# Optimization experiments

Hardware: AMD Instinct MI355X
Metric: run time of the kernel (lower is better)

Reference implementation:

```python
import jax, jax.numpy as jnp
import numpy as np

FILTER_SIZE = 4  # DAIN default filter_size


def _grid(H, W, dtype):
    Y, X = jnp.meshgrid(jnp.arange(H, dtype=dtype), jnp.arange(W, dtype=dtype), indexing='ij')
    return X, Y


def depth_flow_project(flow, depth_inv):
    """DepthFlowProjectionModule: forward-splat -flow, weighted by inverse depth,
    onto the 4 integer neighbors of the flow target, then normalize.
    flow: (B,2,H,W), depth_inv: (B,1,H,W) -> (B,2,H,W) projected flow at time t."""
    B, _, H, W = flow.shape
    X, Y = _grid(H, W, flow.dtype)
    x2 = X[None] + flow[:, 0]
    y2 = Y[None] + flow[:, 1]
    xL = jnp.floor(x2).astype(jnp.int32)
    yT = jnp.floor(y2).astype(jnp.int32)
    d = depth_inv[:, 0]                                            # (B,H,W)
    b_off = (jnp.arange(B, dtype=jnp.int32) * (H * W))[:, None, None]
    fvals = jnp.stack([flow[:, 0], flow[:, 1]], axis=-1).reshape(-1, 2)  # (BHW,2)
    acc = jnp.zeros((B * H * W, 2), flow.dtype)
    cnt = jnp.zeros((B * H * W,), flow.dtype)
    for dy in (0, 1):
        for dx in (0, 1):
            xi = xL + dx
            yi = yT + dy
            valid = (xi >= 0) & (xi < W) & (yi >= 0) & (yi < H)
            idx = (b_off + jnp.clip(yi, 0, H - 1) * W + jnp.clip(xi, 0, W - 1)).reshape(-1)
            w = jnp.where(valid, d, 0.0).reshape(-1)
            acc = acc.at[idx].add(-fvals * w[:, None])
            cnt = cnt.at[idx].add(w)
    cnt_safe = jnp.where(cnt > 0, cnt, 1.0)
    out = jnp.where((cnt > 0)[:, None], acc / cnt_safe[:, None], 0.0)
    return out.reshape(B, H, W, 2).transpose(0, 3, 1, 2)


def _gather(imf, idx, H, W):
    # imf: (B,C,H*W), idx: (B,H,W) int32 -> (B,C,H,W)
    B, C, _ = imf.shape
    g = jax.vmap(lambda m, i: m[:, i])(imf, idx.reshape(B, -1))
    return g.reshape(B, C, H, W)


def filter_interpolate(im, offset, filt):
    """FilterInterpolationModule: per-pixel 4x4 adaptive filter applied at the
    backward-warp location x+u, y+v; each tap is sampled bilinearly at
    (x2 + fi - 1, y2 + fj - 1) and weighted by filt[:, fj*4+fi]."""
    B, C, H, W = im.shape
    X, Y = _grid(H, W, im.dtype)
    x2 = X[None] + offset[:, 0]
    y2 = Y[None] + offset[:, 1]
    valid = (x2 >= 0) & (x2 <= W - 1) & (y2 >= 0) & (y2 <= H - 1)
    xLf = jnp.floor(x2)
    yTf = jnp.floor(y2)
    alpha = (x2 - xLf)[:, None]                                    # (B,1,H,W)
    beta = (y2 - yTf)[:, None]
    xL = xLf.astype(jnp.int32)
    yT = yTf.astype(jnp.int32)
    imf = im.reshape(B, C, H * W)
    half = FILTER_SIZE // 2 - 1  # = 1: window starts at floor - 1
    acc = jnp.zeros_like(im)
    for fj in range(FILTER_SIZE):
        for fi in range(FILTER_SIZE):
            xi = jnp.clip(xL + fi - half, 0, W - 1)
            yi = jnp.clip(yT + fj - half, 0, H - 1)
            xi1 = jnp.clip(xi + 1, 0, W - 1)
            yi1 = jnp.clip(yi + 1, 0, H - 1)
            tl = _gather(imf, yi * W + xi, H, W)
            tr = _gather(imf, yi * W + xi1, H, W)
            bl = _gather(imf, yi1 * W + xi, H, W)
            br = _gather(imf, yi1 * W + xi1, H, W)
            samp = ((1 - alpha) * (1 - beta) * tl + alpha * (1 - beta) * tr
                    + (1 - alpha) * beta * bl + alpha * beta * br)
            acc = acc + filt[:, fj * FILTER_SIZE + fi][:, None] * samp
    return jnp.where(valid[:, None], acc, 0.0)


def setup_inputs() -> dict:
    key = jax.random.key(0)
    ks = jax.random.split(key, 10)
    B, H, W = 2, 192, 320
    CTX = 3 * 64 + 3  # ctx_ch hardcoded in DAIN.__init__
    im0 = jax.random.uniform(ks[0], (B, 3, H, W), jnp.float32)
    im2 = jax.random.uniform(ks[1], (B, 3, H, W), jnp.float32)
    ctx0 = jax.random.normal(ks[2], (B, CTX, H, W), jnp.float32)
    ctx2 = jax.random.normal(ks[3], (B, CTX, H, W), jnp.float32)
    flow01 = jax.random.normal(ks[4], (B, 2, H, W), jnp.float32) * 4.0
    flow10 = jax.random.normal(ks[5], (B, 2, H, W), jnp.float32) * 4.0
    depth0_inv = jax.random.uniform(ks[6], (B, 1, H, W), jnp.float32) + 1e-6
    depth1_inv = jax.random.uniform(ks[7], (B, 1, H, W), jnp.float32) + 1e-6
    filt0 = jax.random.uniform(ks[8], (B, FILTER_SIZE ** 2, H, W), jnp.float32)
    filt1 = jax.random.uniform(ks[9], (B, FILTER_SIZE ** 2, H, W), jnp.float32)
    return {"im0": im0, "im2": im2, "ctx0": ctx0, "ctx2": ctx2,
            "flow01": flow01, "flow10": flow10,
            "depth0_inv": depth0_inv, "depth1_inv": depth1_inv,
            "filt0": filt0, "filt1": filt1}


def reference(im0, im2, ctx0, ctx2, flow01, flow10, depth0_inv, depth1_inv, filt0, filt1):
    # STEP: FlowProject (depth-aware forward warping of the PWC flows to time t)
    off0 = depth_flow_project(flow01, depth0_inv)
    off1 = depth_flow_project(flow10, depth1_inv)
    # STEP: FilterInterpolate on frames (adaptive-filter backward warp) + blend
    ref0 = filter_interpolate(im0, off0, filt0)
    ref2 = filter_interpolate(im2, off1, filt1)
    cur_output = ref0 / 2.0 + ref2 / 2.0
    # STEP: FilterInterpolate_ctx on context features (offsets/filters detached in torch)
    ctx0_w = filter_interpolate(ctx0, jax.lax.stop_gradient(off0), jax.lax.stop_gradient(filt0))
    ctx2_w = filter_interpolate(ctx2, jax.lax.stop_gradient(off1), jax.lax.stop_gradient(filt1))
    return (cur_output, ref0, ref2, ctx0_w, ctx2_w, off0, off1)
```

## Files before the change

### kernel.cpp

```cpp
#include <hip/hip_runtime.h>
#include <hip/hip_fp16.h>
#include <math.h>

#define B   2
#define H   192
#define W   320
#define HW  (H * W)
#define BHW (B * HW)
#define CTX 195
#define CH  198

#define OFS_CUR   0
#define OFS_REF0  (3 * BHW)
#define OFS_REF2  (6 * BHW)
#define OFS_CTX0  (9 * BHW)
#define OFS_CTX2  (9 * BHW + CTX * BHW)
#define OFS_OFF0  (9 * BHW + 2 * CTX * BHW)
#define OFS_OFF1  (OFS_OFF0 + 2 * BHW)

#define TSZ    ((size_t)2 * B * HW * CH)
#define NTB    (2 * B * (HW / 64))
#define LDSW   199
#define NPXB   32
#define NTHR   512
#define NCHK   (HW / NPXB)
#define NBLK2  (2 * B * NCHK)

#define F_NCH   33
#define F_NGRP  6
#define F_TX    32
#define F_TY    8
#define F_NTX   (W / F_TX)
#define F_NTY   (H / F_TY)
#define F_NTILE (F_NTX * F_NTY * B)
#define F_NBLK  (F_NTILE * F_NGRP * 2)

typedef float f4a __attribute__((ext_vector_type(4), aligned(4)));
typedef _Float16 h4 __attribute__((ext_vector_type(4), aligned(4)));

__device__ __forceinline__ int iclip(int v, int lo, int hi) {
    return v < lo ? lo : (v > hi ? hi : v);
}


__global__ __launch_bounds__(256) void splat_kernel(
    const float* __restrict__ flow0, const float* __restrict__ flow1,
    const float* __restrict__ dep0,  const float* __restrict__ dep1,
    float* __restrict__ acc4)
{
    int tid = blockIdx.x * blockDim.x + threadIdx.x;
    if (tid >= 2 * BHW) return;
    int s   = tid / BHW;
    int p   = tid - s * BHW;
    int b   = p / HW;
    int pix = p - b * HW;
    int y   = pix / W;
    int x   = pix - y * W;

    const float* flow = s ? flow1 : flow0;
    const float* dep  = s ? dep1  : dep0;
    float fx = flow[(b * 2 + 0) * HW + pix];
    float fy = flow[(b * 2 + 1) * HW + pix];
    float d  = dep[b * HW + pix];

    int xL = (int)floorf((float)x + fx);
    int yT = (int)floorf((float)y + fy);

    float* ab = acc4 + (size_t)(s * B + b) * HW * 4;

    float wx = -fx * d;
    float wy = -fy * d;
    #pragma unroll
    for (int dy = 0; dy < 2; dy++) {
        #pragma unroll
        for (int dx = 0; dx < 2; dx++) {
            int xi = xL + dx;
            int yi = yT + dy;
            if (xi >= 0 && xi < W && yi >= 0 && yi < H) {
                float* q = ab + (size_t)(yi * W + xi) * 4;
                atomicAdd(q + 0, wx);
                atomicAdd(q + 1, wy);
                atomicAdd(q + 2, d);
            }
        }
    }
}

__global__ __launch_bounds__(256) void norm_kernel(
    float* __restrict__ out, const float* __restrict__ acc4)
{
    int tid = blockIdx.x * blockDim.x + threadIdx.x;
    if (tid >= 2 * BHW) return;
    int s   = tid / BHW;
    int p   = tid - s * BHW;
    int b   = p / HW;
    int pix = p - b * HW;

    const float* q = acc4 + ((size_t)(s * B + b) * HW + pix) * 4;
    float ax = q[0], ay = q[1], c = q[2];
    float* acc = out + (s ? OFS_OFF1 : OFS_OFF0) + b * 2 * HW;
    if (c > 0.0f) {
        acc[pix]      = ax / c;
        acc[HW + pix] = ay / c;
    } else {
        acc[pix]      = 0.0f;
        acc[HW + pix] = 0.0f;
    }
}

__global__ __launch_bounds__(256) void cur_kernel(float* __restrict__ out)
{
    int i = blockIdx.x * blockDim.x + threadIdx.x;
    if (i < 3 * BHW)
        out[OFS_CUR + i] = 0.5f * (out[OFS_REF0 + i] + out[OFS_REF2 + i]);
}


__global__ __launch_bounds__(256) void transpose_kernel(
    const float* __restrict__ im0,  const float* __restrict__ im2,
    const float* __restrict__ ctx0, const float* __restrict__ ctx2,
    _Float16* __restrict__ T)
{
    __shared__ float lds[64 * LDSW];
    int lin   = blockIdx.x;
    int chunk = lin % (HW / 64);
    int rest  = lin / (HW / 64);
    int b = rest % B;
    int s = rest / B;
    int pix0 = chunk * 64;

    const float* im  = s ? im2  : im0;
    const float* ctx = s ? ctx2 : ctx0;

    for (int j = (int)threadIdx.x; j < CH * 64; j += 256) {
        int c = j >> 6;
        int p = j & 63;
        const float* src = (c < 3) ? im + (b * 3 + c) * HW
                                   : ctx + (b * CTX + (c - 3)) * HW;
        lds[p * LDSW + c] = src[pix0 + p];
    }
    __syncthreads();
    _Float16* Tb = T + ((size_t)((s * B + b) * HW + pix0)) * CH;
    for (int j = (int)threadIdx.x; j < CH * 64; j += 256) {
        int p = j / CH;
        int c = j - p * CH;
        Tb[(size_t)p * CH + c] = (_Float16)lds[p * LDSW + c];
    }
}

__global__ __launch_bounds__(NTHR) void interp_t_kernel(
    const _Float16* __restrict__ T,
    const float* __restrict__ filt0, const float* __restrict__ filt1,
    float* __restrict__ out)
{
    __shared__ float fwl[NPXB * 17];
    __shared__ float mwl[NPXB * 25];
    __shared__ float geof[NPXB * 6];
    __shared__ int   geoi[NPXB * 4];
    __shared__ float outb[NPXB * 199];

    int lin = blockIdx.x;
    int newlin = (lin & 7) * (NBLK2 / 8) + (lin >> 3);
    int chunk = newlin % NCHK;
    int rest  = newlin / NCHK;
    int b = rest % B;
    int s = rest / B;
    int px0 = chunk * NPXB;
    int y0  = px0 / W;
    int x0  = px0 - y0 * W;

    const float* off  = out + (s ? OFS_OFF1 : OFS_OFF0) + b * 2 * HW;
    const float* filt = (s ? filt1 : filt0) + b * 16 * HW;
    const _Float16* Tb = T + (size_t)(s * B + b) * HW * CH;

    int t = (int)threadIdx.x;

    for (int idx = t; idx < 16 * NPXB; idx += NTHR) {
        int tap = idx >> 5, p = idx & 31;
        fwl[p * 17 + tap] = filt[tap * HW + px0 + p];
    }
    if (t < NPXB) {
        int p = t;
        float ox = off[px0 + p];
        float oy = off[HW + px0 + p];
        float x2 = (float)(x0 + p) + ox;
        float y2 = (float)y0 + oy;
        bool valid = (x2 >= 0.0f) && (x2 <= (float)(W - 1)) &&
                     (y2 >= 0.0f) && (y2 <= (float)(H - 1));
        float xLf = floorf(x2), yTf = floorf(y2);
        float al = x2 - xLf, be = y2 - yTf;
        int xL = (int)xLf, yT = (int)yTf;
        bool interior = valid && (xL >= 1) && (xL <= W - 4) &&
                                 (yT >= 1) && (yT <= H - 4);
        geof[p * 6 + 0] = valid ? (1.0f - al) * (1.0f - be) : 0.0f;
        geof[p * 6 + 1] = valid ? al * (1.0f - be) : 0.0f;
        geof[p * 6 + 2] = valid ? (1.0f - al) * be : 0.0f;
        geof[p * 6 + 3] = valid ? al * be : 0.0f;
        geoi[p * 4 + 0] = valid ? (interior ? 1 : 2) : 0;
        geoi[p * 4 + 1] = xL;
        geoi[p * 4 + 2] = yT;
    }
    __syncthreads();
    for (int idx = t; idx < 25 * NPXB; idx += NTHR) {
        int p = idx / 25, rc = idx - p * 25;
        int r = rc / 5, c = rc - r * 5;
        float a00 = geof[p * 6 + 0], a10 = geof[p * 6 + 1];
        float a01 = geof[p * 6 + 2], a11 = geof[p * 6 + 3];
        const float* fw = &fwl[p * 17];
        float v = 0.0f;
        if (r < 4 && c < 4)   v += a00 * fw[r * 4 + c];
        if (r < 4 && c >= 1)  v += a10 * fw[r * 4 + c - 1];
        if (r >= 1 && c < 4)  v += a01 * fw[(r - 1) * 4 + c];
        if (r >= 1 && c >= 1) v += a11 * fw[(r - 1) * 4 + c - 1];
        mwl[p * 25 + rc] = v;
    }
    __syncthreads();

    int wave = t >> 6, lane = t & 63;
    int lcl = lane < 49 ? lane : 49;
    int cc0 = 4 * lcl;
    int nwr = lane < 49 ? 4 : (lane == 49 ? 2 : 0);

    #pragma unroll
    for (int pi = 0; pi < 4; pi++) {
        int p = wave * 4 + pi;
        int flag = geoi[p * 4];
        float acc0 = 0.0f, acc1 = 0.0f, acc2 = 0.0f, acc3 = 0.0f;
        if (flag == 1) {
            int xL = geoi[p * 4 + 1], yT = geoi[p * 4 + 2];
            const _Float16* basep =
                Tb + ((size_t)(yT - 1) * W + (xL - 1)) * CH + cc0;
            #pragma unroll
            for (int r = 0; r < 5; r++) {
                #pragma unroll
                for (int cc = 0; cc < 5; cc++) {
                    h4 v = *(const h4*)(basep + ((size_t)r * W + cc) * CH);
                    float wgt = mwl[p * 25 + r * 5 + cc];
                    acc0 = fmaf(wgt, (float)v.x, acc0);
                    acc1 = fmaf(wgt, (float)v.y, acc1);
                    acc2 = fmaf(wgt, (float)v.z, acc2);
                    acc3 = fmaf(wgt, (float)v.w, acc3);
                }
            }
        } else if (flag == 2) {
            int xL = geoi[p * 4 + 1], yT = geoi[p * 4 + 2];
            float a00 = geof[p * 6 + 0], a10 = geof[p * 6 + 1];
            float a01 = geof[p * 6 + 2], a11 = geof[p * 6 + 3];
            int xi[4], xi1[4], yi[4], yi1[4];
            #pragma unroll
            for (int f = 0; f < 4; f++) {
                int a = iclip(xL + f - 1, 0, W - 1);
                xi[f]  = a;
                xi1[f] = a + 1 > W - 1 ? W - 1 : a + 1;
                int bb = iclip(yT + f - 1, 0, H - 1);
                yi[f]  = bb;
                yi1[f] = bb + 1 > H - 1 ? H - 1 : bb + 1;
            }
            #pragma unroll
            for (int fj = 0; fj < 4; fj++) {
                #pragma unroll
                for (int fi = 0; fi < 4; fi++) {
                    const _Float16* ptl = Tb + ((size_t)yi[fj]  * W + xi[fi])  * CH + cc0;
                    const _Float16* ptr_ = Tb + ((size_t)yi[fj]  * W + xi1[fi]) * CH + cc0;
                    const _Float16* pbl = Tb + ((size_t)yi1[fj] * W + xi[fi])  * CH + cc0;
                    const _Float16* pbr = Tb + ((size_t)yi1[fj] * W + xi1[fi]) * CH + cc0;
                    h4 tl = *(const h4*)ptl;
                    h4 tr = *(const h4*)ptr_;
                    h4 bl = *(const h4*)pbl;
                    h4 br = *(const h4*)pbr;
                    float wgt = fwl[p * 17 + fj * 4 + fi];
                    acc0 = fmaf(wgt, a00*(float)tl.x + a10*(float)tr.x + a01*(float)bl.x + a11*(float)br.x, acc0);
                    acc1 = fmaf(wgt, a00*(float)tl.y + a10*(float)tr.y + a01*(float)bl.y + a11*(float)br.y, acc1);
                    acc2 = fmaf(wgt, a00*(float)tl.z + a10*(float)tr.z + a01*(float)bl.z + a11*(float)br.z, acc2);
                    acc3 = fmaf(wgt, a00*(float)tl.w + a10*(float)tr.w + a01*(float)bl.w + a11*(float)br.w, acc3);
                }
            }
        }
        float* ob = &outb[p * 199 + cc0];
        if (nwr == 4) { ob[0] = acc0; ob[1] = acc1; ob[2] = acc2; ob[3] = acc3; }
        else if (nwr == 2) { ob[0] = acc0; ob[1] = acc1; }
    }

    __syncthreads();
    for (int idx = t; idx < CH * NPXB; idx += NTHR) {
        int c = idx >> 5;
        int p = idx & 31;
        float v = outb[p * 199 + c];
        if (c < 3)
            out[(s ? OFS_REF2 : OFS_REF0) + (b * 3 + c) * HW + px0 + p] = v;
        else
            __builtin_nontemporal_store(
                v, &out[(s ? OFS_CTX2 : OFS_CTX0) + (b * CTX + (c - 3)) * HW + px0 + p]);
    }
}


#define VBODY(PLANE, STORE)                                            \
    {                                                                  \
        const float* p0 = (PLANE) + base;                              \
        float acc = 0.0f;                                              \
        _Pragma("unroll")                                              \
        for (int r = 0; r < 5; r++) {                                  \
            const float* row = p0 + r * W;                             \
            f4a v0 = *(const f4a*)row;                                 \
            float v4 = row[4];                                         \
            acc = fmaf(mw[r][0], v0.x, acc);                           \
            acc = fmaf(mw[r][1], v0.y, acc);                           \
            acc = fmaf(mw[r][2], v0.z, acc);                           \
            acc = fmaf(mw[r][3], v0.w, acc);                           \
            acc = fmaf(mw[r][4], v4,   acc);                           \
        }                                                              \
        STORE;                                                         \
    }

#define BBODY(PLANE, STORE)                                            \
    {                                                                  \
        const float* plane = (PLANE);                                  \
        float acc = 0.0f;                                              \
        _Pragma("unroll")                                              \
        for (int fj = 0; fj < 4; fj++) {                               \
            const float* rT = plane + yi[fj]  * W;                     \
            const float* rB = plane + yi1[fj] * W;                     \
            _Pragma("unroll")                                          \
            for (int fi = 0; fi < 4; fi++) {                           \
                float samp = a00 * rT[xi[fi]] + a10 * rT[xi1[fi]]      \
                           + a01 * rB[xi[fi]] + a11 * rB[xi1[fi]];     \
                acc = fmaf(fw[fj * 4 + fi], samp, acc);                \
            }                                                          \
        }                                                              \
        STORE;                                                         \
    }

__global__ __launch_bounds__(256) void interp_f_kernel(
    const float* __restrict__ im0,   const float* __restrict__ im2,
    const float* __restrict__ ctx0,  const float* __restrict__ ctx2,
    const float* __restrict__ filt0, const float* __restrict__ filt1,
    float* __restrict__ out)
{
    int lin = blockIdx.x + F_NTILE * (blockIdx.y + F_NGRP * blockIdx.z);
    int newlin = (lin & 7) * (F_NBLK / 8) + (lin >> 3);
    int tile = newlin % F_NTILE;
    int rest = newlin / F_NTILE;
    int g = rest % F_NGRP;
    int s = rest / F_NGRP;
    int b  = tile / (F_NTX * F_NTY);
    int t2 = tile % (F_NTX * F_NTY);
    int x = (t2 % F_NTX) * F_TX + ((int)threadIdx.x % F_TX);
    int y = (t2 / F_NTX) * F_TY + ((int)threadIdx.x / F_TX);
    int pix = y * W + x;

    const float* off = out + (s ? OFS_OFF1 : OFS_OFF0) + b * 2 * HW;
    float ox = off[pix];
    float oy = off[HW + pix];
    float x2 = (float)x + ox;
    float y2 = (float)y + oy;

    bool valid = (x2 >= 0.0f) && (x2 <= (float)(W - 1)) &&
                 (y2 >= 0.0f) && (y2 <= (float)(H - 1));

    const float* imsrc  = s ? im2  : im0;
    const float* ctxsrc = s ? ctx2 : ctx0;
    float* oim  = out + (s ? OFS_REF2 : OFS_REF0) + b * 3 * HW + pix;
    float* octx = out + (s ? OFS_CTX2 : OFS_CTX0) + b * CTX * HW + pix;

    int c0 = g * F_NCH, c1 = c0 + F_NCH;
    int imEnd  = c1 < 3 ? c1 : 3;
    int ctxBeg = c0 > 3 ? c0 : 3;

    if (!valid) {
        for (int c = c0; c < imEnd; c++) oim[c * HW] = 0.0f;
        for (int c = ctxBeg; c < c1; c++)
            __builtin_nontemporal_store(0.0f, &octx[(c - 3) * HW]);
        return;
    }

    float xLf = floorf(x2), yTf = floorf(y2);
    float alpha = x2 - xLf, beta = y2 - yTf;
    int xL = (int)xLf, yT = (int)yTf;

    const float* filt = (s ? filt1 : filt0) + b * 16 * HW + pix;
    float fw[16];
    #pragma unroll
    for (int t = 0; t < 16; t++) fw[t] = filt[t * HW];

    float a00 = (1.0f - alpha) * (1.0f - beta);
    float a10 = alpha * (1.0f - beta);
    float a01 = (1.0f - alpha) * beta;
    float a11 = alpha * beta;

    bool interior = (xL >= 1) && (xL <= W - 4) && (yT >= 1) && (yT <= H - 4);

    if (interior) {
        float mw[5][5];
        #pragma unroll
        for (int r = 0; r < 5; r++) {
            #pragma unroll
            for (int c = 0; c < 5; c++) {
                float v = 0.0f;
                if (r < 4 && c < 4)   v += a00 * fw[r * 4 + c];
                if (r < 4 && c >= 1)  v += a10 * fw[r * 4 + c - 1];
                if (r >= 1 && c < 4)  v += a01 * fw[(r - 1) * 4 + c];
                if (r >= 1 && c >= 1) v += a11 * fw[(r - 1) * 4 + c - 1];
                mw[r][c] = v;
            }
        }
        int base = (yT - 1) * W + (xL - 1);
        for (int c = c0; c < imEnd; c++)
            VBODY(imsrc + (b * 3 + c) * HW, oim[c * HW] = acc)
        #pragma unroll 2
        for (int c = ctxBeg; c < c1; c++)
            VBODY(ctxsrc + (b * CTX + (c - 3)) * HW,
                  __builtin_nontemporal_store(acc, &octx[(c - 3) * HW]))
    } else {
        int xi[4], xi1[4], yi[4], yi1[4];
        #pragma unroll
        for (int f = 0; f < 4; f++) {
            int a = iclip(xL + f - 1, 0, W - 1);
            xi[f]  = a;
            xi1[f] = a + 1 > W - 1 ? W - 1 : a + 1;
            int bb = iclip(yT + f - 1, 0, H - 1);
            yi[f]  = bb;
            yi1[f] = bb + 1 > H - 1 ? H - 1 : bb + 1;
        }
        for (int c = c0; c < imEnd; c++)
            BBODY(imsrc + (b * 3 + c) * HW, oim[c * HW] = acc)
        for (int c = ctxBeg; c < c1; c++)
            BBODY(ctxsrc + (b * CTX + (c - 3)) * HW,
                  __builtin_nontemporal_store(acc, &octx[(c - 3) * HW]))
    }
}


extern "C" void kernel_launch(void* const* d_in, const int* in_sizes, int n_in,
                              void* d_out, int out_size, void* d_ws, size_t ws_size,
                              hipStream_t stream)
{
    const float* im0    = (const float*)d_in[0];
    const float* im2    = (const float*)d_in[1];
    const float* ctx0   = (const float*)d_in[2];
    const float* ctx2   = (const float*)d_in[3];
    const float* flow01 = (const float*)d_in[4];
    const float* flow10 = (const float*)d_in[5];
    const float* dep0   = (const float*)d_in[6];
    const float* dep1   = (const float*)d_in[7];
    const float* filt0  = (const float*)d_in[8];
    const float* filt1  = (const float*)d_in[9];

    float* out = (float*)d_out;

    size_t acc4_bytes = (size_t)2 * BHW * 4 * sizeof(float);
    size_t need = acc4_bytes + TSZ * sizeof(_Float16);
    bool use_t = ws_size >= need;

    float* acc4 = (float*)d_ws;
    _Float16* T = (_Float16*)((char*)d_ws + acc4_bytes);

    hipMemsetAsync(acc4, 0, acc4_bytes, stream);

    dim3 blk(256);
    splat_kernel<<<dim3((2 * BHW + 255) / 256), blk, 0, stream>>>(
        flow01, flow10, dep0, dep1, acc4);
    norm_kernel<<<dim3((2 * BHW + 255) / 256), blk, 0, stream>>>(out, acc4);

    if (use_t) {
        transpose_kernel<<<dim3(NTB), blk, 0, stream>>>(im0, im2, ctx0, ctx2, T);
        interp_t_kernel<<<dim3(NBLK2), dim3(NTHR), 0, stream>>>(T, filt0, filt1, out);
    } else {
        dim3 igrid(F_NTILE, F_NGRP, 2);
        interp_f_kernel<<<igrid, blk, 0, stream>>>(
            im0, im2, ctx0, ctx2, filt0, filt1, out);
    }

    cur_kernel<<<dim3((3 * BHW + 255) / 256), blk, 0, stream>>>(out);
}
```

Measured before the change: 517.0 us.

## Unify interior/border interp paths with 5x5 merged weights and 8-wide half loads

```diff
diff --git a/kernel.cpp b/kernel.cpp
--- a/kernel.cpp
+++ b/kernel.cpp
@@ -36,7 +36,7 @@
 #define F_NBLK  (F_NTILE * F_NGRP * 2)
 
 typedef float f4a __attribute__((ext_vector_type(4), aligned(4)));
-typedef _Float16 h4 __attribute__((ext_vector_type(4), aligned(4)));
+typedef _Float16 h8 __attribute__((ext_vector_type(8), aligned(4)));
 
 __device__ __forceinline__ int iclip(int v, int lo, int hi) {
     return v < lo ? lo : (v > hi ? hi : v);
@@ -155,8 +155,10 @@
 {
     __shared__ float fwl[NPXB * 17];
     __shared__ float mwl[NPXB * 25];
-    __shared__ float geof[NPXB * 6];
-    __shared__ int   geoi[NPXB * 4];
+    __shared__ float geoA[NPXB * 4];
+    __shared__ int   geoC[NPXB * 4];
+    __shared__ int   rofs[NPXB * 5];
+    __shared__ int   cofs[NPXB * 5];
     __shared__ float outb[NPXB * 199];
 
     int lin = blockIdx.x;
@@ -175,6 +177,7 @@
 
     int t = (int)threadIdx.x;
 
+    for (int idx = t; idx < 25 * NPXB; idx += NTHR) mwl[idx] = 0.0f;
     for (int idx = t; idx < 16 * NPXB; idx += NTHR) {
         int tap = idx >> 5, p = idx & 31;
         fwl[p * 17 + tap] = filt[tap * HW + px0 + p];
@@ -189,96 +192,93 @@
                      (y2 >= 0.0f) && (y2 <= (float)(H - 1));
         float xLf = floorf(x2), yTf = floorf(y2);
         float al = x2 - xLf, be = y2 - yTf;
-        int xL = (int)xLf, yT = (int)yTf;
-        bool interior = valid && (xL >= 1) && (xL <= W - 4) &&
-                                 (yT >= 1) && (yT <= H - 4);
-        geof[p * 6 + 0] = valid ? (1.0f - al) * (1.0f - be) : 0.0f;
-        geof[p * 6 + 1] = valid ? al * (1.0f - be) : 0.0f;
-        geof[p * 6 + 2] = valid ? (1.0f - al) * be : 0.0f;
-        geof[p * 6 + 3] = valid ? al * be : 0.0f;
-        geoi[p * 4 + 0] = valid ? (interior ? 1 : 2) : 0;
-        geoi[p * 4 + 1] = xL;
-        geoi[p * 4 + 2] = yT;
+        int xL = valid ? (int)xLf : 1;
+        int yT = valid ? (int)yTf : 1;
+        geoA[p * 4 + 0] = valid ? (1.0f - al) * (1.0f - be) : 0.0f;
+        geoA[p * 4 + 1] = valid ? al * (1.0f - be) : 0.0f;
+        geoA[p * 4 + 2] = valid ? (1.0f - al) * be : 0.0f;
+        geoA[p * 4 + 3] = valid ? al * be : 0.0f;
+        geoC[p * 4 + 0] = xL;
+        geoC[p * 4 + 1] = yT;
+        geoC[p * 4 + 2] = xL - 1 > 0 ? xL - 1 : 0;
+        geoC[p * 4 + 3] = yT - 1 > 0 ? yT - 1 : 0;
     }
     __syncthreads();
-    for (int idx = t; idx < 25 * NPXB; idx += NTHR) {
-        int p = idx / 25, rc = idx - p * 25;
-        int r = rc / 5, c = rc - r * 5;
-        float a00 = geof[p * 6 + 0], a10 = geof[p * 6 + 1];
-        float a01 = geof[p * 6 + 2], a11 = geof[p * 6 + 3];
-        const float* fw = &fwl[p * 17];
-        float v = 0.0f;
-        if (r < 4 && c < 4)   v += a00 * fw[r * 4 + c];
-        if (r < 4 && c >= 1)  v += a10 * fw[r * 4 + c - 1];
-        if (r >= 1 && c < 4)  v += a01 * fw[(r - 1) * 4 + c];
-        if (r >= 1 && c >= 1) v += a11 * fw[(r - 1) * 4 + c - 1];
-        mwl[p * 25 + rc] = v;
+
+    for (int idx = t; idx < 2 * 5 * NPXB; idx += NTHR) {
+        if (idx < 5 * NPXB) {
+            int p = idx / 5, r = idx - p * 5;
+            int by = geoC[p * 4 + 3];
+            int yr = by + r; if (yr > H - 1) yr = H - 1;
+            rofs[p * 5 + r] = yr * (W * CH);
+        } else {
+            int j = idx - 5 * NPXB;
+            int p = j / 5, c = j - p * 5;
+            int bx = geoC[p * 4 + 2];
+            int xc = bx + c; if (xc > W - 1) xc = W - 1;
+            cofs[p * 5 + c] = xc * CH;
+        }
+    }
+
+    {
+        int p = t >> 4, tap = t & 15;
+        int fi = tap & 3, fj = tap >> 2;
+        int xL = geoC[p * 4 + 0], yT = geoC[p * 4 + 1];
+        int bx = geoC[p * 4 + 2], by = geoC[p * 4 + 3];
+        float fw = fwl[p * 17 + tap];
+        float a00 = geoA[p * 4 + 0], a10 = geoA[p * 4 + 1];
+        float a01 = geoA[p * 4 + 2], a11 = geoA[p * 4 + 3];
+        int xi  = iclip(xL + fi - 1, 0, W - 1);
+        int xi1 = xi + 1 > W - 1 ? W - 1 : xi + 1;
+        int yi  = iclip(yT + fj - 1, 0, H - 1);
+        int yi1 = yi + 1 > H - 1 ? H - 1 : yi + 1;
+        float* mwp = &mwl[p * 25];
+        atomicAdd(&mwp[(yi  - by) * 5 + (xi  - bx)], fw * a00);
+        atomicAdd(&mwp[(yi  - by) * 5 + (xi1 - bx)], fw * a10);
+        atomicAdd(&mwp[(yi1 - by) * 5 + (xi  - bx)], fw * a01);
+        atomicAdd(&mwp[(yi1 - by) * 5 + (xi1 - bx)], fw * a11);
     }
     __syncthreads();
 
     int wave = t >> 6, lane = t & 63;
-    int lcl = lane < 49 ? lane : 49;
-    int cc0 = 4 * lcl;
-    int nwr = lane < 49 ? 4 : (lane == 49 ? 2 : 0);
+    int grp = lane >> 5;
+    int li  = lane & 31;
+    int lcl = li < 24 ? li : 24;
+    int ch0 = lcl * 8;
 
     #pragma unroll
-    for (int pi = 0; pi < 4; pi++) {
-        int p = wave * 4 + pi;
-        int flag = geoi[p * 4];
-        float acc0 = 0.0f, acc1 = 0.0f, acc2 = 0.0f, acc3 = 0.0f;
-        if (flag == 1) {
-            int xL = geoi[p * 4 + 1], yT = geoi[p * 4 + 2];
-            const _Float16* basep =
-                Tb + ((size_t)(yT - 1) * W + (xL - 1)) * CH + cc0;
+    for (int pr = 0; pr < 2; pr++) {
+        int p = wave * 4 + pr * 2 + grp;
+        const float* mwp = &mwl[p * 25];
+        const int* rp = &rofs[p * 5];
+        const int* cp = &cofs[p * 5];
+        const _Float16* bp = Tb + ch0;
+        float a0 = 0, a1 = 0, a2 = 0, a3 = 0, a4 = 0, a5 = 0, a6 = 0, a7 = 0;
+        #pragma unroll
+        for (int r = 0; r < 5; r++) {
+            const _Float16* rowp = bp + rp[r];
             #pragma unroll
-            for (int r = 0; r < 5; r++) {
-                #pragma unroll
-                for (int cc = 0; cc < 5; cc++) {
-                    h4 v = *(const h4*)(basep + ((size_t)r * W + cc) * CH);
-                    float wgt = mwl[p * 25 + r * 5 + cc];
-                    acc0 = fmaf(wgt, (float)v.x, acc0);
-                    acc1 = fmaf(wgt, (float)v.y, acc1);
-                    acc2 = fmaf(wgt, (float)v.z, acc2);
-                    acc3 = fmaf(wgt, (float)v.w, acc3);
-                }
+            for (int c = 0; c < 5; c++) {
+                h8 v = *(const h8*)(rowp + cp[c]);
+                float w = mwp[r * 5 + c];
+                a0 = fmaf(w, (float)v[0], a0);
+                a1 = fmaf(w, (float)v[1], a1);
+                a2 = fmaf(w, (float)v[2], a2);
+                a3 = fmaf(w, (float)v[3], a3);
+                a4 = fmaf(w, (float)v[4], a4);
+                a5 = fmaf(w, (float)v[5], a5);
+                a6 = fmaf(w, (float)v[6], a6);
+                a7 = fmaf(w, (float)v[7], a7);
             }
-        } else if (flag == 2) {
-            int xL = geoi[p * 4 + 1], yT = geoi[p * 4 + 2];
-            float a00 = geof[p * 6 + 0], a10 = geof[p * 6 + 1];
-            float a01 = geof[p * 6 + 2], a11 = geof[p * 6 + 3];
-            int xi[4], xi1[4], yi[4], yi1[4];
-            #pragma unroll
-            for (int f = 0; f < 4; f++) {
-                int a = iclip(xL + f - 1, 0, W - 1);
-                xi[f]  = a;
-                xi1[f] = a + 1 > W - 1 ? W - 1 : a + 1;
-                int bb = iclip(yT + f - 1, 0, H - 1);
-                yi[f]  = bb;
-                yi1[f] = bb + 1 > H - 1 ? H - 1 : bb + 1;
-            }
-            #pragma unroll
-            for (int fj = 0; fj < 4; fj++) {
-                #pragma unroll
-                for (int fi = 0; fi < 4; fi++) {
-                    const _Float16* ptl = Tb + ((size_t)yi[fj]  * W + xi[fi])  * CH + cc0;
-                    const _Float16* ptr_ = Tb + ((size_t)yi[fj]  * W + xi1[fi]) * CH + cc0;
-                    const _Float16* pbl = Tb + ((size_t)yi1[fj] * W + xi[fi])  * CH + cc0;
-                    const _Float16* pbr = Tb + ((size_t)yi1[fj] * W + xi1[fi]) * CH + cc0;
-                    h4 tl = *(const h4*)ptl;
-                    h4 tr = *(const h4*)ptr_;
-                    h4 bl = *(const h4*)pbl;
-                    h4 br = *(const h4*)pbr;
-                    float wgt = fwl[p * 17 + fj * 4 + fi];
-                    acc0 = fmaf(wgt, a00*(float)tl.x + a10*(float)tr.x + a01*(float)bl.x + a11*(float)br.x, acc0);
-                    acc1 = fmaf(wgt, a00*(float)tl.y + a10*(float)tr.y + a01*(float)bl.y + a11*(float)br.y, acc1);
-                    acc2 = fmaf(wgt, a00*(float)tl.z + a10*(float)tr.z + a01*(float)bl.z + a11*(float)br.z, acc2);
-                    acc3 = fmaf(wgt, a00*(float)tl.w + a10*(float)tr.w + a01*(float)bl.w + a11*(float)br.w, acc3);
-                }
-            }
-        }
-        float* ob = &outb[p * 199 + cc0];
-        if (nwr == 4) { ob[0] = acc0; ob[1] = acc1; ob[2] = acc2; ob[3] = acc3; }
-        else if (nwr == 2) { ob[0] = acc0; ob[1] = acc1; }
+        }
+        float* ob = &outb[p * 199 + ch0];
+        if (li < 24) {
+            ob[0] = a0; ob[1] = a1; ob[2] = a2; ob[3] = a3;
+            ob[4] = a4; ob[5] = a5; ob[6] = a6; ob[7] = a7;
+        } else if (li == 24) {
+            ob[0] = a0; ob[1] = a1; ob[2] = a2;
+            ob[3] = a3; ob[4] = a4; ob[5] = a5;
+        }
     }
 
     __syncthreads();
@@ -448,12 +448,13 @@
 
     float* out = (float*)d_out;
 
+    size_t t_bytes    = TSZ * sizeof(_Float16);
     size_t acc4_bytes = (size_t)2 * BHW * 4 * sizeof(float);
-    size_t need = acc4_bytes + TSZ * sizeof(_Float16);
+    size_t need = t_bytes + acc4_bytes;
     bool use_t = ws_size >= need;
 
-    float* acc4 = (float*)d_ws;
-    _Float16* T = (_Float16*)((char*)d_ws + acc4_bytes);
+    _Float16* T = (_Float16*)d_ws;
+    float* acc4 = use_t ? (float*)((char*)d_ws + t_bytes) : (float*)d_ws;
 
     hipMemsetAsync(acc4, 0, acc4_bytes, stream);
 
```

Result: slower. 531.2 us (+2.7%).
